# Kernel optimization log

Hardware: AMD Instinct MI355X
Metric: run time of the kernel (lower is better)

## Reference

```python
import jax, jax.numpy as jnp
import numpy as np

HORIZON = 60
HID = 128

def setup_inputs() -> dict:
    key = jax.random.key(0)
    ks = jax.random.split(key, 7)
    B, D, O = 16384, 256, 3
    s_ih = 1.0 / np.sqrt(HID)
    return {
        "x": jax.random.normal(ks[0], (B, D), jnp.float32),
        "W_ih": jax.random.normal(ks[1], (3 * HID, D), jnp.float32) * s_ih,
        "W_hh": jax.random.normal(ks[2], (3 * HID, HID), jnp.float32) * s_ih,
        "b_ih": jax.random.normal(ks[3], (3 * HID,), jnp.float32) * s_ih,
        "b_hh": jax.random.normal(ks[4], (3 * HID,), jnp.float32) * s_ih,
        "W_out": jax.random.normal(ks[5], (O, HID), jnp.float32) * s_ih,
        "b_out": jax.random.normal(ks[6], (O,), jnp.float32) * s_ih,
    }

def reference(x, W_ih, W_hh, b_ih, b_hh, W_out, b_out):
    # Input is identical at every timestep -> precompute input projection once.
    B = x.shape[0]
    gi = x @ W_ih.T + b_ih                      # [B, 3H]
    gi_r, gi_z, gi_n = jnp.split(gi, 3, axis=-1)

    def step(h, _):
        gh = h @ W_hh.T + b_hh                  # [B, 3H]
        gh_r, gh_z, gh_n = jnp.split(gh, 3, axis=-1)
        r = jax.nn.sigmoid(gi_r + gh_r)
        z = jax.nn.sigmoid(gi_z + gh_z)
        n = jnp.tanh(gi_n + r * gh_n)
        h_new = (1.0 - z) * n + z * h           # torch GRU update
        return h_new, h_new

    h0 = jnp.zeros((B, HID), x.dtype)
    _, hs = jax.lax.scan(step, h0, None, length=HORIZON)   # [T, B, H]
    out = jnp.einsum('tbh,oh->bto', hs, W_out) + b_out     # [B, T, O]
    return out
```

## Files before the change

### kernel.cpp

```cpp
#include <hip/hip_runtime.h>


typedef __attribute__((ext_vector_type(8))) short short8;
typedef __attribute__((ext_vector_type(4))) float f32x4;

#define MFMA16(a, b, c) __builtin_amdgcn_mfma_f32_16x16x32_bf16((a), (b), (c), 0, 0, 0)

__device__ __forceinline__ short f2bf(float x) {
    union { float f; unsigned u; } v; v.f = x;
    unsigned r = v.u + 0x7FFFu + ((v.u >> 16) & 1u);
    return (short)(r >> 16);
}

__device__ __forceinline__ unsigned cvtpk(float lo, float hi) {
    unsigned d;
    asm("v_cvt_pk_bf16_f32 %0, %1, %2" : "=v"(d) : "v"(lo), "v"(hi));
    return d;
}

__device__ __forceinline__ short8 cvt8(const float* __restrict__ p) {
    f32x4 a = *(const f32x4*)p;
    f32x4 b = *(const f32x4*)(p + 4);
    short8 r;
    r[0] = f2bf(a[0]); r[1] = f2bf(a[1]); r[2] = f2bf(a[2]); r[3] = f2bf(a[3]);
    r[4] = f2bf(b[0]); r[5] = f2bf(b[1]); r[6] = f2bf(b[2]); r[7] = f2bf(b[3]);
    return r;
}
__device__ __forceinline__ short8 cvt8s(const float* __restrict__ p, float s) {
    f32x4 a = *(const f32x4*)p;
    f32x4 b = *(const f32x4*)(p + 4);
    short8 r;
    r[0] = f2bf(a[0] * s); r[1] = f2bf(a[1] * s); r[2] = f2bf(a[2] * s); r[3] = f2bf(a[3] * s);
    r[4] = f2bf(b[0] * s); r[5] = f2bf(b[1] * s); r[6] = f2bf(b[2] * s); r[7] = f2bf(b[3] * s);
    return r;
}

__global__ __launch_bounds__(512, 4) void gru_traj_kernel(
    const float* __restrict__ x,
    const float* __restrict__ W_ih,
    const float* __restrict__ W_hh,
    const float* __restrict__ b_ih,
    const float* __restrict__ b_hh,
    const float* __restrict__ W_out,
    const float* __restrict__ b_out,
    float* __restrict__ out)
{
    const int tid  = threadIdx.x;
    const int wid  = tid >> 6;
    const int lane = tid & 63;
    const int l15  = lane & 15;
    const int l4   = lane >> 4;
    const int b0   = blockIdx.x << 5;
    const int hb   = wid << 4;

    const float SCL  = -1.442695041f;
    const float SCL2 = -2.885390082f;

    __shared__ short hbuf[2][32 * 128];
    __shared__ float gibuf[2 * 8 * 2 * 256];
    __shared__ short wobuf[3 * 136];

    {
        int* z = (int*)hbuf[0];
        #pragma unroll
        for (int i = 0; i < 4; ++i) z[tid + i * 512] = 0;
    }
    if (tid < 384) wobuf[(tid >> 7) * 136 + (tid & 127)] = f2bf(W_out[tid]);

    short8 wfrag[3][4];
    #pragma unroll
    for (int kt = 0; kt < 4; ++kt) {
        wfrag[0][kt] = cvt8s(W_hh + (size_t)(      hb + l15) * 128 + kt * 32 + l4 * 8, SCL);
        wfrag[1][kt] = cvt8s(W_hh + (size_t)(128 + hb + l15) * 128 + kt * 32 + l4 * 8, SCL);
        wfrag[2][kt] = cvt8 (W_hh + (size_t)(256 + hb + l15) * 128 + kt * 32 + l4 * 8);
    }

    const int bbase = hb + l4 * 4;
    const f32x4 bR4 = (*(const f32x4*)(b_ih + bbase)       + *(const f32x4*)(b_hh + bbase))       * SCL;
    const f32x4 bZ4 = (*(const f32x4*)(b_ih + 128 + bbase) + *(const f32x4*)(b_hh + 128 + bbase)) * SCL;
    const f32x4 bNi = *(const f32x4*)(b_ih + 256 + bbase);
    const f32x4 bNh = *(const f32x4*)(b_hh + 256 + bbase);
    const float bo0 = b_out[0], bo1 = b_out[1], bo2 = b_out[2];

    f32x4 giN[2];
    {
        f32x4 initR[2], initZ[2];
        #pragma unroll
        for (int q = 0; q < 2; ++q) { initR[q] = bR4; initZ[q] = bZ4; giN[q] = bNi; }
        #pragma unroll
        for (int kt = 0; kt < 8; ++kt) {
            short8 a0 = cvt8s(W_ih + (size_t)(      hb + l15) * 256 + kt * 32 + l4 * 8, SCL);
            short8 a1 = cvt8s(W_ih + (size_t)(128 + hb + l15) * 256 + kt * 32 + l4 * 8, SCL);
            short8 a2 = cvt8 (W_ih + (size_t)(256 + hb + l15) * 256 + kt * 32 + l4 * 8);
            #pragma unroll
            for (int q = 0; q < 2; ++q) {
                short8 bx = cvt8(x + (size_t)(b0 + q * 16 + l15) * 256 + kt * 32 + l4 * 8);
                initR[q] = MFMA16(a0, bx, initR[q]);
                initZ[q] = MFMA16(a1, bx, initZ[q]);
                giN [q] = MFMA16(a2, bx, giN [q]);
            }
        }
        #pragma unroll
        for (int q = 0; q < 2; ++q) {
            *(f32x4*)(gibuf + ((0 * 8 + wid) * 2 + q) * 256 + lane * 4) = initR[q];
            *(f32x4*)(gibuf + ((1 * 8 + wid) * 2 + q) * 256 + lane * 4) = initZ[q];
        }
    }

    float hq[2][4];
    #pragma unroll
    for (int q = 0; q < 2; ++q)
        #pragma unroll
        for (int r = 0; r < 4; ++r) hq[q][r] = 0.f;

    const int s8 = (wid << 2) | l4;

    __syncthreads();

    #pragma unroll 2
    for (int t = 0; t < 60; ++t) {
        const short* rb = hbuf[t & 1];
        short*       wb = hbuf[(t & 1) ^ 1];
        #pragma unroll
        for (int q = 0; q < 2; ++q) {
            short8 af[4];
            #pragma unroll
            for (int kt = 0; kt < 4; ++kt)
                af[kt] = *(const short8*)(rb + (q * 16 + l15) * 128 + (((kt * 4 + l4) ^ l15) & 15) * 8);

            if (t > 0 && wid == ((q + t) & 7)) {
                f32x4 oa = (f32x4){0.f, 0.f, 0.f, 0.f};
                #pragma unroll
                for (int kt = 0; kt < 4; ++kt) {
                    short8 wo = {0, 0, 0, 0, 0, 0, 0, 0};
                    if (l15 < 3) wo = *(const short8*)(wobuf + l15 * 136 + kt * 32 + l4 * 8);
                    oa = MFMA16(wo, af[kt], oa);
                }
                if (l4 == 0) {
                    float* op = out + (size_t)(b0 + q * 16 + l15) * 180 + (t - 1) * 3;
                    op[0] = oa[0] + bo0; op[1] = oa[1] + bo1; op[2] = oa[2] + bo2;
                }
            }

            f32x4 aR = *(const f32x4*)(gibuf + ((0 * 8 + wid) * 2 + q) * 256 + lane * 4);
            f32x4 aZ = *(const f32x4*)(gibuf + ((1 * 8 + wid) * 2 + q) * 256 + lane * 4);
            f32x4 aN = bNh;
            #pragma unroll
            for (int kt = 0; kt < 4; ++kt) {
                aR = MFMA16(wfrag[0][kt], af[kt], aR);
                aZ = MFMA16(wfrag[1][kt], af[kt], aZ);
                aN = MFMA16(wfrag[2][kt], af[kt], aN);
            }
            float hn[4];
            #pragma unroll
            for (int r = 0; r < 4; ++r) {
                float eA = __builtin_amdgcn_exp2f(aR[r]);
                float eB = __builtin_amdgcn_exp2f(aZ[r]);
                float A  = 1.0f + eA, Bv = 1.0f + eB;
                float R  = __builtin_amdgcn_rcpf(A * Bv);
                float rr = R * Bv;
                float zz = R * A;
                float sn = fmaf(rr, aN[r], giN[q][r]);
                float eC = __builtin_amdgcn_exp2f(sn * SCL2);
                float nn = fmaf(2.0f, __builtin_amdgcn_rcpf(1.0f + eC), -1.0f);
                hn[r] = fmaf(zz, hq[q][r] - nn, nn);
                hq[q][r] = hn[r];
            }
            uint2 pk;
            pk.x = cvtpk(hn[0], hn[1]);
            pk.y = cvtpk(hn[2], hn[3]);
            *(uint2*)(wb + (q * 16 + l15) * 128 + (((s8 >> 1) ^ l15) & 15) * 8 + (s8 & 1) * 4) = pk;
        }
        __syncthreads();
    }

    if (wid < 2) {
        const int q = wid;
        const short* rb = hbuf[0];
        f32x4 oa = (f32x4){0.f, 0.f, 0.f, 0.f};
        #pragma unroll
        for (int kt = 0; kt < 4; ++kt) {
            short8 af = *(const short8*)(rb + (q * 16 + l15) * 128 + (((kt * 4 + l4) ^ l15) & 15) * 8);
            short8 wo = {0, 0, 0, 0, 0, 0, 0, 0};
            if (l15 < 3) wo = *(const short8*)(wobuf + l15 * 136 + kt * 32 + l4 * 8);
            oa = MFMA16(wo, af, oa);
        }
        if (l4 == 0) {
            float* op = out + (size_t)(b0 + q * 16 + l15) * 180 + 59 * 3;
            op[0] = oa[0] + bo0; op[1] = oa[1] + bo1; op[2] = oa[2] + bo2;
        }
    }
}

extern "C" void kernel_launch(void* const* d_in, const int* in_sizes, int n_in,
                              void* d_out, int out_size, void* d_ws, size_t ws_size,
                              hipStream_t stream) {
    const float* x     = (const float*)d_in[0];
    const float* W_ih  = (const float*)d_in[1];
    const float* W_hh  = (const float*)d_in[2];
    const float* b_ih  = (const float*)d_in[3];
    const float* b_hh  = (const float*)d_in[4];
    const float* W_out = (const float*)d_in[5];
    const float* b_out = (const float*)d_in[6];
    float* out = (float*)d_out;

    const int B = in_sizes[0] / 256;
    hipLaunchKernelGGL(gru_traj_kernel, dim3(B / 32), dim3(512), 0, stream,
                       x, W_ih, W_hh, b_ih, b_hh, W_out, b_out, out);
}
```

Before: 167.3 us.

## Halve batch tile per block to 16 rows and keep gate inputs in registers

Each block now handles 16 batch rows instead of 32, doubling the grid to B/16 blocks. With only one 16-row group per wave, the precomputed R/Z input-gate projections stay in registers instead of being spilled to and reloaded from a shared-memory buffer every step, which also shrinks LDS use. This spreads the sequential 60-step recurrence across more blocks and removes per-step LDS gate loads. The cost is that each block reloads and converts W_hh/W_ih for half as much work, and there is less independent MFMA work per wave to hide latency between barriers.

```diff
diff --git a/kernel.cpp b/kernel.cpp
--- a/kernel.cpp
+++ b/kernel.cpp
@@ -50,20 +50,18 @@
     const int lane = tid & 63;
     const int l15  = lane & 15;
     const int l4   = lane >> 4;
-    const int b0   = blockIdx.x << 5;
+    const int b0   = blockIdx.x << 4;
     const int hb   = wid << 4;
 
     const float SCL  = -1.442695041f;
     const float SCL2 = -2.885390082f;
 
-    __shared__ short hbuf[2][32 * 128];
-    __shared__ float gibuf[2 * 8 * 2 * 256];
+    __shared__ short hbuf[2][16 * 128];
     __shared__ short wobuf[3 * 136];
 
     {
         int* z = (int*)hbuf[0];
-        #pragma unroll
-        for (int i = 0; i < 4; ++i) z[tid + i * 512] = 0;
+        z[tid] = 0; z[tid + 512] = 0;
     }
     if (tid < 384) wobuf[(tid >> 7) * 136 + (tid & 127)] = f2bf(W_out[tid]);
 
@@ -76,43 +74,21 @@
     }
 
     const int bbase = hb + l4 * 4;
-    const f32x4 bR4 = (*(const f32x4*)(b_ih + bbase)       + *(const f32x4*)(b_hh + bbase))       * SCL;
-    const f32x4 bZ4 = (*(const f32x4*)(b_ih + 128 + bbase) + *(const f32x4*)(b_hh + 128 + bbase)) * SCL;
-    const f32x4 bNi = *(const f32x4*)(b_ih + 256 + bbase);
     const f32x4 bNh = *(const f32x4*)(b_hh + 256 + bbase);
     const float bo0 = b_out[0], bo1 = b_out[1], bo2 = b_out[2];
 
-    f32x4 giN[2];
-    {
-        f32x4 initR[2], initZ[2];
-        #pragma unroll
-        for (int q = 0; q < 2; ++q) { initR[q] = bR4; initZ[q] = bZ4; giN[q] = bNi; }
-        #pragma unroll
-        for (int kt = 0; kt < 8; ++kt) {
-            short8 a0 = cvt8s(W_ih + (size_t)(      hb + l15) * 256 + kt * 32 + l4 * 8, SCL);
-            short8 a1 = cvt8s(W_ih + (size_t)(128 + hb + l15) * 256 + kt * 32 + l4 * 8, SCL);
-            short8 a2 = cvt8 (W_ih + (size_t)(256 + hb + l15) * 256 + kt * 32 + l4 * 8);
-            #pragma unroll
-            for (int q = 0; q < 2; ++q) {
-                short8 bx = cvt8(x + (size_t)(b0 + q * 16 + l15) * 256 + kt * 32 + l4 * 8);
-                initR[q] = MFMA16(a0, bx, initR[q]);
-                initZ[q] = MFMA16(a1, bx, initZ[q]);
-                giN [q] = MFMA16(a2, bx, giN [q]);
-            }
-        }
-        #pragma unroll
-        for (int q = 0; q < 2; ++q) {
-            *(f32x4*)(gibuf + ((0 * 8 + wid) * 2 + q) * 256 + lane * 4) = initR[q];
-            *(f32x4*)(gibuf + ((1 * 8 + wid) * 2 + q) * 256 + lane * 4) = initZ[q];
-        }
+    f32x4 initR = (*(const f32x4*)(b_ih + bbase)       + *(const f32x4*)(b_hh + bbase))       * SCL;
+    f32x4 initZ = (*(const f32x4*)(b_ih + 128 + bbase) + *(const f32x4*)(b_hh + 128 + bbase)) * SCL;
+    f32x4 giN   = *(const f32x4*)(b_ih + 256 + bbase);
+    #pragma unroll
+    for (int kt = 0; kt < 8; ++kt) {
+        short8 bx = cvt8(x + (size_t)(b0 + l15) * 256 + kt * 32 + l4 * 8);
+        initR = MFMA16(cvt8s(W_ih + (size_t)(      hb + l15) * 256 + kt * 32 + l4 * 8, SCL), bx, initR);
+        initZ = MFMA16(cvt8s(W_ih + (size_t)(128 + hb + l15) * 256 + kt * 32 + l4 * 8, SCL), bx, initZ);
+        giN   = MFMA16(cvt8 (W_ih + (size_t)(256 + hb + l15) * 256 + kt * 32 + l4 * 8),      bx, giN);
     }
 
-    float hq[2][4];
-    #pragma unroll
-    for (int q = 0; q < 2; ++q)
-        #pragma unroll
-        for (int r = 0; r < 4; ++r) hq[q][r] = 0.f;
-
+    float hq[4] = {0.f, 0.f, 0.f, 0.f};
     const int s8 = (wid << 2) | l4;
 
     __syncthreads();
@@ -121,72 +97,68 @@
     for (int t = 0; t < 60; ++t) {
         const short* rb = hbuf[t & 1];
         short*       wb = hbuf[(t & 1) ^ 1];
+
+        short8 af[4];
         #pragma unroll
-        for (int q = 0; q < 2; ++q) {
-            short8 af[4];
-            #pragma unroll
-            for (int kt = 0; kt < 4; ++kt)
-                af[kt] = *(const short8*)(rb + (q * 16 + l15) * 128 + (((kt * 4 + l4) ^ l15) & 15) * 8);
+        for (int kt = 0; kt < 4; ++kt)
+            af[kt] = *(const short8*)(rb + l15 * 128 + (((kt * 4 + l4) ^ l15) & 15) * 8);
 
-            if (t > 0 && wid == ((q + t) & 7)) {
-                f32x4 oa = (f32x4){0.f, 0.f, 0.f, 0.f};
-                #pragma unroll
-                for (int kt = 0; kt < 4; ++kt) {
-                    short8 wo = {0, 0, 0, 0, 0, 0, 0, 0};
-                    if (l15 < 3) wo = *(const short8*)(wobuf + l15 * 136 + kt * 32 + l4 * 8);
-                    oa = MFMA16(wo, af[kt], oa);
-                }
-                if (l4 == 0) {
-                    float* op = out + (size_t)(b0 + q * 16 + l15) * 180 + (t - 1) * 3;
-                    op[0] = oa[0] + bo0; op[1] = oa[1] + bo1; op[2] = oa[2] + bo2;
-                }
-            }
-
-            f32x4 aR = *(const f32x4*)(gibuf + ((0 * 8 + wid) * 2 + q) * 256 + lane * 4);
-            f32x4 aZ = *(const f32x4*)(gibuf + ((1 * 8 + wid) * 2 + q) * 256 + lane * 4);
-            f32x4 aN = bNh;
+        if (t > 0 && wid == (t & 7)) {
+            f32x4 oa = (f32x4){0.f, 0.f, 0.f, 0.f};
             #pragma unroll
             for (int kt = 0; kt < 4; ++kt) {
-                aR = MFMA16(wfrag[0][kt], af[kt], aR);
-                aZ = MFMA16(wfrag[1][kt], af[kt], aZ);
-                aN = MFMA16(wfrag[2][kt], af[kt], aN);
+                short8 wo = {0, 0, 0, 0, 0, 0, 0, 0};
+                if (l15 < 3) wo = *(const short8*)(wobuf + l15 * 136 + kt * 32 + l4 * 8);
+                oa = MFMA16(wo, af[kt], oa);
             }
-            float hn[4];
-            #pragma unroll
-            for (int r = 0; r < 4; ++r) {
-                float eA = __builtin_amdgcn_exp2f(aR[r]);
-                float eB = __builtin_amdgcn_exp2f(aZ[r]);
-                float A  = 1.0f + eA, Bv = 1.0f + eB;
-                float R  = __builtin_amdgcn_rcpf(A * Bv);
-                float rr = R * Bv;
-                float zz = R * A;
-                float sn = fmaf(rr, aN[r], giN[q][r]);
-                float eC = __builtin_amdgcn_exp2f(sn * SCL2);
-                float nn = fmaf(2.0f, __builtin_amdgcn_rcpf(1.0f + eC), -1.0f);
-                hn[r] = fmaf(zz, hq[q][r] - nn, nn);
-                hq[q][r] = hn[r];
+            if (l4 == 0) {
+                float* op = out + (size_t)(b0 + l15) * 180 + (t - 1) * 3;
+                op[0] = oa[0] + bo0; op[1] = oa[1] + bo1; op[2] = oa[2] + bo2;
             }
-            uint2 pk;
-            pk.x = cvtpk(hn[0], hn[1]);
-            pk.y = cvtpk(hn[2], hn[3]);
-            *(uint2*)(wb + (q * 16 + l15) * 128 + (((s8 >> 1) ^ l15) & 15) * 8 + (s8 & 1) * 4) = pk;
         }
+
+        f32x4 aR = initR, aZ = initZ, aN = bNh;
+        #pragma unroll
+        for (int kt = 0; kt < 4; ++kt) {
+            aR = MFMA16(wfrag[0][kt], af[kt], aR);
+            aZ = MFMA16(wfrag[1][kt], af[kt], aZ);
+            aN = MFMA16(wfrag[2][kt], af[kt], aN);
+        }
+        float hn[4];
+        #pragma unroll
+        for (int r = 0; r < 4; ++r) {
+            float eA = __builtin_amdgcn_exp2f(aR[r]);
+            float eB = __builtin_amdgcn_exp2f(aZ[r]);
+            float A  = 1.0f + eA, Bv = 1.0f + eB;
+            float R  = __builtin_amdgcn_rcpf(A * Bv);
+            float rr = R * Bv;
+            float zz = R * A;
+            float sn = fmaf(rr, aN[r], giN[r]);
+            float eC = __builtin_amdgcn_exp2f(sn * SCL2);
+            float nn = fmaf(2.0f, __builtin_amdgcn_rcpf(1.0f + eC), -1.0f);
+            hn[r] = fmaf(zz, hq[r] - nn, nn);
+            hq[r] = hn[r];
+        }
+        uint2 pk;
+        pk.x = cvtpk(hn[0], hn[1]);
+        pk.y = cvtpk(hn[2], hn[3]);
+        *(uint2*)(wb + l15 * 128 + (((s8 >> 1) ^ l15) & 15) * 8 + (s8 & 1) * 4) = pk;
+
         __syncthreads();
     }
 
-    if (wid < 2) {
-        const int q = wid;
+    if (wid == 4) {
         const short* rb = hbuf[0];
         f32x4 oa = (f32x4){0.f, 0.f, 0.f, 0.f};
         #pragma unroll
         for (int kt = 0; kt < 4; ++kt) {
-            short8 af = *(const short8*)(rb + (q * 16 + l15) * 128 + (((kt * 4 + l4) ^ l15) & 15) * 8);
+            short8 af = *(const short8*)(rb + l15 * 128 + (((kt * 4 + l4) ^ l15) & 15) * 8);
             short8 wo = {0, 0, 0, 0, 0, 0, 0, 0};
             if (l15 < 3) wo = *(const short8*)(wobuf + l15 * 136 + kt * 32 + l4 * 8);
             oa = MFMA16(wo, af, oa);
         }
         if (l4 == 0) {
-            float* op = out + (size_t)(b0 + q * 16 + l15) * 180 + 59 * 3;
+            float* op = out + (size_t)(b0 + l15) * 180 + 59 * 3;
             op[0] = oa[0] + bo0; op[1] = oa[1] + bo1; op[2] = oa[2] + bo2;
         }
     }
@@ -205,6 +177,6 @@
     float* out = (float*)d_out;
 
     const int B = in_sizes[0] / 256;
-    hipLaunchKernelGGL(gru_traj_kernel, dim3(B / 32), dim3(512), 0, stream,
+    hipLaunchKernelGGL(gru_traj_kernel, dim3(B / 16), dim3(512), 0, stream,
                        x, W_ih, W_hh, b_ih, b_hh, W_out, b_out, out);
 }
```

Result: slower. 208.1 us (+24.4%).

## Double batch rows per block, keep input gates in registers, prefetch h fragments

Applied to the files above, without the earlier changes.

Each block now handles 64 batch rows instead of 32, which halves the grid and the number of per-block W_hh/W_ih fragment loads and conversions. The precomputed input-gate projections stay in registers instead of being reread from LDS each step, which removes the gibuf buffer. The LDS reads of the next 16-row h tile are software-pipelined with the MFMAs on the current tile, and the swizzled offsets are precomputed. The cost is higher register pressure, which is why the occupancy target in launch bounds drops from 4 to 2. There are also fewer blocks per CU and more serial work per timestep between barriers.

```diff
diff --git a/kernel.cpp b/kernel.cpp
--- a/kernel.cpp
+++ b/kernel.cpp
@@ -35,7 +35,7 @@
     return r;
 }
 
-__global__ __launch_bounds__(512, 4) void gru_traj_kernel(
+__global__ __launch_bounds__(512, 2) void gru_traj_kernel(
     const float* __restrict__ x,
     const float* __restrict__ W_ih,
     const float* __restrict__ W_hh,
@@ -50,20 +50,19 @@
     const int lane = tid & 63;
     const int l15  = lane & 15;
     const int l4   = lane >> 4;
-    const int b0   = blockIdx.x << 5;
+    const int b0   = blockIdx.x << 6;
     const int hb   = wid << 4;
 
     const float SCL  = -1.442695041f;
     const float SCL2 = -2.885390082f;
 
-    __shared__ short hbuf[2][32 * 128];
-    __shared__ float gibuf[2 * 8 * 2 * 256];
+    __shared__ short hbuf[2][64 * 128];
     __shared__ short wobuf[3 * 136];
 
     {
         int* z = (int*)hbuf[0];
         #pragma unroll
-        for (int i = 0; i < 4; ++i) z[tid + i * 512] = 0;
+        for (int i = 0; i < 8; ++i) z[tid + i * 512] = 0;
     }
     if (tid < 384) wobuf[(tid >> 7) * 136 + (tid & 127)] = f2bf(W_out[tid]);
 
@@ -82,51 +81,63 @@
     const f32x4 bNh = *(const f32x4*)(b_hh + 256 + bbase);
     const float bo0 = b_out[0], bo1 = b_out[1], bo2 = b_out[2];
 
-    f32x4 giN[2];
-    {
-        f32x4 initR[2], initZ[2];
-        #pragma unroll
-        for (int q = 0; q < 2; ++q) { initR[q] = bR4; initZ[q] = bZ4; giN[q] = bNi; }
-        #pragma unroll
-        for (int kt = 0; kt < 8; ++kt) {
-            short8 a0 = cvt8s(W_ih + (size_t)(      hb + l15) * 256 + kt * 32 + l4 * 8, SCL);
-            short8 a1 = cvt8s(W_ih + (size_t)(128 + hb + l15) * 256 + kt * 32 + l4 * 8, SCL);
-            short8 a2 = cvt8 (W_ih + (size_t)(256 + hb + l15) * 256 + kt * 32 + l4 * 8);
-            #pragma unroll
-            for (int q = 0; q < 2; ++q) {
-                short8 bx = cvt8(x + (size_t)(b0 + q * 16 + l15) * 256 + kt * 32 + l4 * 8);
-                initR[q] = MFMA16(a0, bx, initR[q]);
-                initZ[q] = MFMA16(a1, bx, initZ[q]);
-                giN [q] = MFMA16(a2, bx, giN [q]);
-            }
-        }
-        #pragma unroll
-        for (int q = 0; q < 2; ++q) {
-            *(f32x4*)(gibuf + ((0 * 8 + wid) * 2 + q) * 256 + lane * 4) = initR[q];
-            *(f32x4*)(gibuf + ((1 * 8 + wid) * 2 + q) * 256 + lane * 4) = initZ[q];
-        }
-    }
-
-    float hq[2][4];
-    #pragma unroll
-    for (int q = 0; q < 2; ++q)
+    f32x4 initR[4], initZ[4], giN[4];
+    #pragma unroll
+    for (int q = 0; q < 4; ++q) { initR[q] = bR4; initZ[q] = bZ4; giN[q] = bNi; }
+    #pragma unroll
+    for (int kt = 0; kt < 8; ++kt) {
+        short8 a0 = cvt8s(W_ih + (size_t)(      hb + l15) * 256 + kt * 32 + l4 * 8, SCL);
+        short8 a1 = cvt8s(W_ih + (size_t)(128 + hb + l15) * 256 + kt * 32 + l4 * 8, SCL);
+        short8 a2 = cvt8 (W_ih + (size_t)(256 + hb + l15) * 256 + kt * 32 + l4 * 8);
+        #pragma unroll
+        for (int q = 0; q < 4; ++q) {
+            short8 bx = cvt8(x + (size_t)(b0 + q * 16 + l15) * 256 + kt * 32 + l4 * 8);
+            initR[q] = MFMA16(a0, bx, initR[q]);
+            initZ[q] = MFMA16(a1, bx, initZ[q]);
+            giN [q] = MFMA16(a2, bx, giN [q]);
+        }
+    }
+
+    float hq[4][4];
+    #pragma unroll
+    for (int q = 0; q < 4; ++q)
         #pragma unroll
         for (int r = 0; r < 4; ++r) hq[q][r] = 0.f;
 
     const int s8 = (wid << 2) | l4;
+    int roff[4];
+    #pragma unroll
+    for (int kt = 0; kt < 4; ++kt)
+        roff[kt] = (l15 * 128 + (((kt * 4 + l4) ^ l15) & 15) * 8) * 2;
+    const int woff = (l15 * 128 + (((s8 >> 1) ^ l15) & 15) * 8 + (s8 & 1) * 4) * 2;
 
     __syncthreads();
 
     #pragma unroll 2
     for (int t = 0; t < 60; ++t) {
-        const short* rb = hbuf[t & 1];
-        short*       wb = hbuf[(t & 1) ^ 1];
-        #pragma unroll
-        for (int q = 0; q < 2; ++q) {
-            short8 af[4];
+        const char* rb = (const char*)hbuf[t & 1];
+        char*       wb = (char*)hbuf[(t & 1) ^ 1];
+
+        short8 afc[4], afn[4];
+        #pragma unroll
+        for (int kt = 0; kt < 4; ++kt)
+            afc[kt] = *(const short8*)(rb + roff[kt]);
+
+        #pragma unroll
+        for (int q = 0; q < 4; ++q) {
+            if (q < 3) {
+                #pragma unroll
+                for (int kt = 0; kt < 4; ++kt)
+                    afn[kt] = *(const short8*)(rb + roff[kt] + (q + 1) * 4096);
+            }
+
+            f32x4 aR = initR[q], aZ = initZ[q], aN = bNh;
             #pragma unroll
-            for (int kt = 0; kt < 4; ++kt)
-                af[kt] = *(const short8*)(rb + (q * 16 + l15) * 128 + (((kt * 4 + l4) ^ l15) & 15) * 8);
+            for (int kt = 0; kt < 4; ++kt) {
+                aR = MFMA16(wfrag[0][kt], afc[kt], aR);
+                aZ = MFMA16(wfrag[1][kt], afc[kt], aZ);
+                aN = MFMA16(wfrag[2][kt], afc[kt], aN);
+            }
 
             if (t > 0 && wid == ((q + t) & 7)) {
                 f32x4 oa = (f32x4){0.f, 0.f, 0.f, 0.f};
@@ -134,7 +145,7 @@
                 for (int kt = 0; kt < 4; ++kt) {
                     short8 wo = {0, 0, 0, 0, 0, 0, 0, 0};
                     if (l15 < 3) wo = *(const short8*)(wobuf + l15 * 136 + kt * 32 + l4 * 8);
-                    oa = MFMA16(wo, af[kt], oa);
+                    oa = MFMA16(wo, afc[kt], oa);
                 }
                 if (l4 == 0) {
                     float* op = out + (size_t)(b0 + q * 16 + l15) * 180 + (t - 1) * 3;
@@ -142,15 +153,6 @@
                 }
             }
 
-            f32x4 aR = *(const f32x4*)(gibuf + ((0 * 8 + wid) * 2 + q) * 256 + lane * 4);
-            f32x4 aZ = *(const f32x4*)(gibuf + ((1 * 8 + wid) * 2 + q) * 256 + lane * 4);
-            f32x4 aN = bNh;
-            #pragma unroll
-            for (int kt = 0; kt < 4; ++kt) {
-                aR = MFMA16(wfrag[0][kt], af[kt], aR);
-                aZ = MFMA16(wfrag[1][kt], af[kt], aZ);
-                aN = MFMA16(wfrag[2][kt], af[kt], aN);
-            }
             float hn[4];
             #pragma unroll
             for (int r = 0; r < 4; ++r) {
@@ -169,18 +171,21 @@
             uint2 pk;
             pk.x = cvtpk(hn[0], hn[1]);
             pk.y = cvtpk(hn[2], hn[3]);
-            *(uint2*)(wb + (q * 16 + l15) * 128 + (((s8 >> 1) ^ l15) & 15) * 8 + (s8 & 1) * 4) = pk;
+            *(uint2*)(wb + woff + q * 4096) = pk;
+
+            #pragma unroll
+            for (int kt = 0; kt < 4; ++kt) afc[kt] = afn[kt];
         }
         __syncthreads();
     }
 
-    if (wid < 2) {
+    if (wid < 4) {
         const int q = wid;
-        const short* rb = hbuf[0];
+        const char* rb = (const char*)hbuf[0];
         f32x4 oa = (f32x4){0.f, 0.f, 0.f, 0.f};
         #pragma unroll
         for (int kt = 0; kt < 4; ++kt) {
-            short8 af = *(const short8*)(rb + (q * 16 + l15) * 128 + (((kt * 4 + l4) ^ l15) & 15) * 8);
+            short8 af = *(const short8*)(rb + roff[kt] + q * 4096);
             short8 wo = {0, 0, 0, 0, 0, 0, 0, 0};
             if (l15 < 3) wo = *(const short8*)(wobuf + l15 * 136 + kt * 32 + l4 * 8);
             oa = MFMA16(wo, af, oa);
@@ -205,6 +210,6 @@
     float* out = (float*)d_out;
 
     const int B = in_sizes[0] / 256;
-    hipLaunchKernelGGL(gru_traj_kernel, dim3(B / 32), dim3(512), 0, stream,
+    hipLaunchKernelGGL(gru_traj_kernel, dim3(B / 64), dim3(512), 0, stream,
                        x, W_ih, W_hh, b_ih, b_hh, W_out, b_out, out);
 }
```

Result: faster. 154.4 us (-7.7%).
